# Performance work log

Measured on AMD Instinct MI355X. Metric: run time of the kernel, lower is better.

The kernel has to match this reference:

```python
import jax, jax.numpy as jnp
import numpy as np

MAXDISP = 21  # default maxDisp from __init__


def _make_kernel():
    # convweights[i,0,:,0:2] = 1/6 ; convweights[i,0,:,i+2] = -1/3 ; bias[i] = i+1
    w = np.zeros((MAXDISP, 1, 3, MAXDISP + 2), dtype=np.float32)
    for i in range(MAXDISP):
        w[i, 0, :, 0:2] = 1.0 / 6.0
        w[i, 0, :, i + 2] = -1.0 / 3.0
    b = np.arange(1, MAXDISP + 1, dtype=np.float32)
    return jnp.asarray(w), jnp.asarray(b)


def _compute_mask(disp, w, b):
    # ReplicationPad2d((left=0, right=maxDisp+1, top=1, bottom=1))
    pad = jnp.pad(disp, ((0, 0), (0, 0), (1, 1), (0, MAXDISP + 1)), mode='edge')
    # conv2d, VALID: output spatial size == input spatial size
    out = jax.lax.conv_general_dilated(
        pad, w, window_strides=(1, 1), padding='VALID',
        dimension_numbers=('NCHW', 'OIHW', 'NCHW'))
    out = jnp.abs(out + b[None, :, None, None])          # [B, maxDisp, H, W]
    mask = jnp.min(out, axis=1, keepdims=True)           # channel-min -> [B,1,H,W]
    return jnp.clip(mask, 0.0, 1.0)


def _forward(dispmap, bsline):
    w, b = _make_kernel()
    maskl = _compute_mask(dispmap, w, b)
    # 'r' direction: flip along width, compute, flip back
    maskr = jnp.flip(_compute_mask(jnp.flip(dispmap, axis=3), w, b), axis=3)
    bs = bsline[:, None, None, None]
    zero = jnp.zeros_like(dispmap)
    # bsline < 0 -> left mask; bsline > 0 -> right mask; else zeros
    return jnp.where(bs < 0, maskl, jnp.where(bs > 0, maskr, zero))


def setup_inputs() -> dict:
    key = jax.random.key(0)
    k1, k2 = jax.random.split(key)
    # disparity-like values in [0, 1)
    dispmap = jax.random.uniform(k1, (8, 1, 384, 1280), dtype=jnp.float32)
    bsline = jax.random.normal(k2, (8,), dtype=jnp.float32)
    return {"dispmap": dispmap, "bsline": bsline}


def reference(dispmap, bsline):
    return _forward(dispmap, bsline)
```

## Files before the change

### kernel.cpp

```cpp
#include <hip/hip_runtime.h>

#define W  1280
#define H  384
#define ND 21
#define BT 320
#define R  4

template <int DIR>
__device__ __forceinline__ void compute_row(const float* __restrict__ Cs,
                                            float* __restrict__ orow, int t) {
    float V[28];
    const float4* p = (const float4*)(Cs + ((DIR > 0) ? 4 * t : 4 * t - 24));
    #pragma unroll
    for (int m = 0; m < 7; m++) {
        float4 f = p[m];
        V[4*m+0] = f.x; V[4*m+1] = f.y; V[4*m+2] = f.z; V[4*m+3] = f.w;
    }
    float Q[24];
    #pragma unroll
    for (int m = 0; m < 24; m++) {
        float k = (DIR > 0) ? (float)(m + 1) : (float)(21 - m);
        Q[m] = k - V[m + 2] * (1.0f / 3.0f);
    }
    float4 o; float* op = &o.x;
    #pragma unroll
    for (int j = 0; j < 4; j++) {
        float base = (DIR > 0) ? (V[j] + V[j+1]) * (1.0f / 6.0f)
                               : (V[24+j] + V[23+j]) * (1.0f / 6.0f);
        float B = (DIR > 0) ? (base - (float)j) : (base + (float)j);
        float m0 = 1e30f;
        #pragma unroll
        for (int i = 0; i < ND; i++)
            m0 = fminf(m0, fabsf(B + Q[j + i]));
        op[j] = fminf(m0, 1.0f);
    }
    ((float4*)orow)[t] = o;
}

template <int DIR>
__device__ __forceinline__ void run_rows(const float* __restrict__ dbase,
                                         float* __restrict__ outb,
                                         float (*Cbuf)[W + 48],
                                         int rs, int t) {
    const bool lp = (t < 24);
    const bool rp = (t >= 32 && t < 56);
    const int  ecol = lp ? 0 : (W - 1);

    int r0 = max(rs - 1, 0);
    float4 a = ((const float4*)(dbase + (size_t)r0       * W))[t];
    float4 b = ((const float4*)(dbase + (size_t)rs       * W))[t];
    float4 c = ((const float4*)(dbase + (size_t)(rs + 1) * W))[t];
    float4 d = {0, 0, 0, 0};
    float ea = 0, eb = 0, ec = 0, ed = 0;
    if (lp || rp) {
        ea = dbase[(size_t)r0       * W + ecol];
        eb = dbase[(size_t)rs       * W + ecol];
        ec = dbase[(size_t)(rs + 1) * W + ecol];
    }

    #pragma unroll
    for (int r = 0; r < R; r++) {
        float* Cs = Cbuf[r & 1] + 24;
        float4 s;
        s.x = a.x + b.x + c.x; s.y = a.y + b.y + c.y;
        s.z = a.z + b.z + c.z; s.w = a.w + b.w + c.w;
        ((float4*)Cs)[t] = s;
        if (lp)      Cs[t - 24]      = ea + eb + ec;
        else if (rp) Cs[W + (t - 32)] = ea + eb + ec;

        if (r + 1 < R) {
            int nr = min(rs + r + 2, H - 1);
            d = ((const float4*)(dbase + (size_t)nr * W))[t];
            if (lp || rp) ed = dbase[(size_t)nr * W + ecol];
        }
        __syncthreads();
        compute_row<DIR>(Cs, outb + (size_t)r * W, t);
        a = b; b = c; c = d;
        ea = eb; eb = ec; ec = ed;
    }
}

__global__ __launch_bounds__(BT) void occl_kernel(const float* __restrict__ disp,
                                                  const float* __restrict__ bsl,
                                                  float* __restrict__ out) {
    int g = blockIdx.x, nb = gridDim.x;
    int id = (nb & 7) ? g : ((g & 7) * (nb >> 3) + (g >> 3));
    const int RB = H / R;
    const int batch = id / RB;
    const int rs = (id % RB) * R;
    const float bs = bsl[batch];
    const int t = threadIdx.x;
    float* outb = out + ((size_t)batch * H + rs) * W;

    if (bs == 0.0f) {
        float4 z = {0, 0, 0, 0};
        #pragma unroll
        for (int r = 0; r < R; r++) ((float4*)(outb + (size_t)r * W))[t] = z;
        return;
    }

    __shared__ float Cbuf[2][W + 48];
    const float* dbase = disp + (size_t)batch * H * W;

    if (bs < 0.0f) run_rows<1>(dbase, outb, Cbuf, rs, t);
    else           run_rows<-1>(dbase, outb, Cbuf, rs, t);
}

extern "C" void kernel_launch(void* const* d_in, const int* in_sizes, int n_in,
                              void* d_out, int out_size, void* d_ws, size_t ws_size,
                              hipStream_t stream) {
    const float* disp = (const float*)d_in[0];
    const float* bsl  = (const float*)d_in[1];
    float* out        = (float*)d_out;
    const int n_batch = in_sizes[1];

    occl_kernel<<<dim3(n_batch * (H / R)), BT, 0, stream>>>(disp, bsl, out);
}
```

Before: 72.69 us.

## Add wave-uniform fast path skipping channel-min when column sums lie in [0,3]

```diff
diff --git a/kernel.cpp b/kernel.cpp
--- a/kernel.cpp
+++ b/kernel.cpp
@@ -6,77 +6,115 @@
 #define BT 320
 #define R  4
 
+
+__device__ __forceinline__ float colsum_g(const float* __restrict__ d,
+                                          int rm, int r0, int rp, int x) {
+    x = min(max(x, 0), W - 1);
+    return d[(size_t)rm * W + x] + d[(size_t)r0 * W + x] + d[(size_t)rp * W + x];
+}
+
 template <int DIR>
-__device__ __forceinline__ void compute_row(const float* __restrict__ Cs,
-                                            float* __restrict__ orow, int t) {
-    float V[28];
-    const float4* p = (const float4*)(Cs + ((DIR > 0) ? 4 * t : 4 * t - 24));
+__device__ __forceinline__ void slow_row(const float* __restrict__ dbase,
+                                         int rm, int r0, int rp,
+                                         float* __restrict__ orow, int t) {
+    float V[26];
+    const int x0 = (DIR > 0) ? 4 * t : 4 * t - 22;
     #pragma unroll
-    for (int m = 0; m < 7; m++) {
-        float4 f = p[m];
-        V[4*m+0] = f.x; V[4*m+1] = f.y; V[4*m+2] = f.z; V[4*m+3] = f.w;
-    }
-    float Q[24];
-    #pragma unroll
-    for (int m = 0; m < 24; m++) {
-        float k = (DIR > 0) ? (float)(m + 1) : (float)(21 - m);
-        Q[m] = k - V[m + 2] * (1.0f / 3.0f);
-    }
+    for (int k = 0; k < 26; k++) V[k] = colsum_g(dbase, rm, r0, rp, x0 + k);
     float4 o; float* op = &o.x;
     #pragma unroll
     for (int j = 0; j < 4; j++) {
-        float base = (DIR > 0) ? (V[j] + V[j+1]) * (1.0f / 6.0f)
-                               : (V[24+j] + V[23+j]) * (1.0f / 6.0f);
-        float B = (DIR > 0) ? (base - (float)j) : (base + (float)j);
+        float base = (DIR > 0) ? (V[j] + V[j + 1]) * (1.0f / 6.0f)
+                               : (V[22 + j] + V[21 + j]) * (1.0f / 6.0f);
         float m0 = 1e30f;
         #pragma unroll
-        for (int i = 0; i < ND; i++)
-            m0 = fminf(m0, fabsf(B + Q[j + i]));
+        for (int i = 0; i < ND; i++) {
+            float Cx = (DIR > 0) ? V[j + 2 + i] : V[20 + j - i];
+            m0 = fminf(m0, fabsf(base + (float)(i + 1) - Cx * (1.0f / 3.0f)));
+        }
         op[j] = fminf(m0, 1.0f);
     }
     ((float4*)orow)[t] = o;
 }
 
 template <int DIR>
+__device__ __forceinline__ void load_row(const float* __restrict__ dbase, int row,
+                                         int t, int lane, int hcol,
+                                         float4& A, float4& B, float4& Hh) {
+    const float4* rp = (const float4*)(dbase + (size_t)row * W);
+    A = rp[t];
+    if (DIR > 0) {
+        B = (t < BT - 1) ? rp[t + 1] : make_float4(A.w, A.w, A.w, A.w);
+    } else {
+        B = (t > 0) ? rp[t - 1] : make_float4(A.x, A.x, A.x, A.x);
+    }
+    if (lane < 6) Hh = rp[hcol >> 2];
+}
+
+template <int DIR>
 __device__ __forceinline__ void run_rows(const float* __restrict__ dbase,
                                          float* __restrict__ outb,
-                                         float (*Cbuf)[W + 48],
                                          int rs, int t) {
-    const bool lp = (t < 24);
-    const bool rp = (t >= 32 && t < 56);
-    const int  ecol = lp ? 0 : (W - 1);
+    const int lane  = t & 63;
+    const int wbase = (t >> 6) << 8;
+    const int hcol = (DIR > 0) ? min(wbase + 256 + 4 * lane, W - 4)
+                               : max(wbase - 24 + 4 * lane, 0);
+
+    float4 aA = {0,0,0,0}, aB = {0,0,0,0}, aH = {0,0,0,0};
+    float4 bA = {0,0,0,0}, bB = {0,0,0,0}, bH = {0,0,0,0};
+    float4 cA = {0,0,0,0}, cB = {0,0,0,0}, cH = {0,0,0,0};
+    float4 dA = {0,0,0,0}, dB = {0,0,0,0}, dH = {0,0,0,0};
 
     int r0 = max(rs - 1, 0);
-    float4 a = ((const float4*)(dbase + (size_t)r0       * W))[t];
-    float4 b = ((const float4*)(dbase + (size_t)rs       * W))[t];
-    float4 c = ((const float4*)(dbase + (size_t)(rs + 1) * W))[t];
-    float4 d = {0, 0, 0, 0};
-    float ea = 0, eb = 0, ec = 0, ed = 0;
-    if (lp || rp) {
-        ea = dbase[(size_t)r0       * W + ecol];
-        eb = dbase[(size_t)rs       * W + ecol];
-        ec = dbase[(size_t)(rs + 1) * W + ecol];
-    }
+    load_row<DIR>(dbase, r0,     t, lane, hcol, aA, aB, aH);
+    load_row<DIR>(dbase, rs,     t, lane, hcol, bA, bB, bH);
+    load_row<DIR>(dbase, rs + 1, t, lane, hcol, cA, cB, cH);
 
     #pragma unroll
     for (int r = 0; r < R; r++) {
-        float* Cs = Cbuf[r & 1] + 24;
-        float4 s;
-        s.x = a.x + b.x + c.x; s.y = a.y + b.y + c.y;
-        s.z = a.z + b.z + c.z; s.w = a.w + b.w + c.w;
-        ((float4*)Cs)[t] = s;
-        if (lp)      Cs[t - 24]      = ea + eb + ec;
-        else if (rp) Cs[W + (t - 32)] = ea + eb + ec;
-
         if (r + 1 < R) {
             int nr = min(rs + r + 2, H - 1);
-            d = ((const float4*)(dbase + (size_t)nr * W))[t];
-            if (lp || rp) ed = dbase[(size_t)nr * W + ecol];
+            load_row<DIR>(dbase, nr, t, lane, hcol, dA, dB, dH);
         }
-        __syncthreads();
-        compute_row<DIR>(Cs, outb + (size_t)r * W, t);
-        a = b; b = c; c = d;
-        ea = eb; eb = ec; ec = ed;
+
+        float SA[4] = {aA.x + bA.x + cA.x, aA.y + bA.y + cA.y,
+                       aA.z + bA.z + cA.z, aA.w + bA.w + cA.w};
+        float SB[4] = {aB.x + bB.x + cB.x, aB.y + bB.y + cB.y,
+                       aB.z + bB.z + cB.z, aB.w + bB.w + cB.w};
+
+        float mx = fmaxf(fmaxf(SA[0], SA[1]), fmaxf(SA[2], SA[3]));
+        float mn = fminf(fminf(SA[0], SA[1]), fminf(SA[2], SA[3]));
+        if (lane < 6) {
+            float h0 = aH.x + bH.x + cH.x, h1 = aH.y + bH.y + cH.y;
+            float h2 = aH.z + bH.z + cH.z, h3 = aH.w + bH.w + cH.w;
+            mx = fmaxf(mx, fmaxf(fmaxf(h0, h1), fmaxf(h2, h3)));
+            mn = fminf(mn, fminf(fminf(h0, h1), fminf(h2, h3)));
+        }
+
+        if (!__any(mx > 3.0f || mn < 0.0f)) {
+            float4 o; float* op = &o.x;
+            if (DIR > 0) {
+                float S[6] = {SA[0], SA[1], SA[2], SA[3], SB[0], SB[1]};
+                #pragma unroll
+                for (int j = 0; j < 4; j++)
+                    op[j] = fminf(fabsf((S[j] + S[j + 1]) * (1.0f / 6.0f)
+                                        - S[j + 2] * (1.0f / 3.0f) + 1.0f), 1.0f);
+            } else {
+                float S[8] = {SB[0], SB[1], SB[2], SB[3], SA[0], SA[1], SA[2], SA[3]};
+                #pragma unroll
+                for (int j = 0; j < 4; j++)
+                    op[j] = fminf(fabsf((S[4 + j] + S[3 + j]) * (1.0f / 6.0f)
+                                        - S[2 + j] * (1.0f / 3.0f) + 1.0f), 1.0f);
+            }
+            ((float4*)(outb + (size_t)r * W))[t] = o;
+        } else {
+            int rm = max(rs + r - 1, 0), rc = rs + r, rp2 = min(rs + r + 1, H - 1);
+            slow_row<DIR>(dbase, rm, rc, rp2, outb + (size_t)r * W, t);
+        }
+
+        aA = bA; aB = bB; aH = bH;
+        bA = cA; bB = cB; bH = cH;
+        cA = dA; cB = dB; cH = dH;
     }
 }
 
@@ -99,11 +137,10 @@
         return;
     }
 
-    __shared__ float Cbuf[2][W + 48];
     const float* dbase = disp + (size_t)batch * H * W;
 
-    if (bs < 0.0f) run_rows<1>(dbase, outb, Cbuf, rs, t);
-    else           run_rows<-1>(dbase, outb, Cbuf, rs, t);
+    if (bs < 0.0f) run_rows<1>(dbase, outb, rs, t);
+    else           run_rows<-1>(dbase, outb, rs, t);
 }
 
 extern "C" void kernel_launch(void* const* d_in, const int* in_sizes, int n_in,
```

After: 74.56 us. 2.6% more time.
